# Kernel tuning notes

Hardware: AMD Instinct MI355X
Metric: run time of the kernel (lower is better)

## Reference

```python
import jax, jax.numpy as jnp
import numpy as np

N_USER = 50000
N_ITEM = 50000
E = 800000
D_IN = 256
H = 4
D_OUT = 32


def setup_inputs() -> dict:
    key = jax.random.key(0)
    ks = jax.random.split(key, 13)
    s = 0.05  # param init scale
    return {
        "feat_user": jax.random.normal(ks[0], (N_USER, D_IN), jnp.float32),
        "feat_item": jax.random.normal(ks[1], (N_ITEM, D_IN), jnp.float32),
        # relation 1: user -> item
        "src_r1": jax.random.randint(ks[2], (E,), 0, N_USER, jnp.int32),
        "dst_r1": jax.random.randint(ks[3], (E,), 0, N_ITEM, jnp.int32),
        # relation 2: item -> user
        "src_r2": jax.random.randint(ks[4], (E,), 0, N_ITEM, jnp.int32),
        "dst_r2": jax.random.randint(ks[5], (E,), 0, N_USER, jnp.int32),
        "fc_r1": jax.random.normal(ks[6], (D_IN, H * D_OUT), jnp.float32) * s,
        "attn_l_r1": jax.random.normal(ks[7], (H, D_OUT), jnp.float32) * s,
        "attn_r_r1": jax.random.normal(ks[8], (H, D_OUT), jnp.float32) * s,
        "fc_r2": jax.random.normal(ks[9], (D_IN, H * D_OUT), jnp.float32) * s,
        "attn_l_r2": jax.random.normal(ks[10], (H, D_OUT), jnp.float32) * s,
        "attn_r_r2": jax.random.normal(ks[11], (H, D_OUT), jnp.float32) * s,
        "loop_weight": jax.random.normal(ks[12], (D_IN, D_OUT), jnp.float32) * s,
    }


def _gat_conv(feat_src, feat_dst, src, dst, fc, attn_l, attn_r, n_dst):
    """DGL-style GATConv: LeakyReLU(0.2) scores, edge softmax over dst, scatter-sum, elu."""
    hs = (feat_src @ fc).reshape(-1, H, D_OUT)  # (Nsrc, H, D)
    hd = (feat_dst @ fc).reshape(-1, H, D_OUT)  # (Ndst, H, D)
    el = jnp.sum(hs * attn_l, axis=-1)  # (Nsrc, H)
    er = jnp.sum(hd * attn_r, axis=-1)  # (Ndst, H)
    e = jax.nn.leaky_relu(el[src] + er[dst], 0.2)  # (E, H)
    # numerically stable segment softmax over dst neighborhoods
    emax = jax.ops.segment_max(e, dst, num_segments=n_dst)  # (Ndst, H)
    emax = jnp.where(jnp.isfinite(emax), emax, 0.0)  # zero-in-degree guard
    ex = jnp.exp(e - emax[dst])  # (E, H)
    denom = jax.ops.segment_sum(ex, dst, num_segments=n_dst)  # (Ndst, H)
    msg = ex[:, :, None] * hs[src]  # (E, H, D)
    agg = jax.ops.segment_sum(msg, dst, num_segments=n_dst)  # (Ndst, H, D)
    out = agg / jnp.maximum(denom, 1e-9)[:, :, None]
    return jax.nn.elu(out)


def reference(feat_user, feat_item, src_r1, dst_r1, src_r2, dst_r2,
              fc_r1, attn_l_r1, attn_r_r1, fc_r2, attn_l_r2, attn_r_r2,
              loop_weight):
    # HeteroGraphConv: each dst ntype receives one relation here (sum-agg trivial)
    h_item = _gat_conv(feat_user, feat_item, src_r1, dst_r1,
                       fc_r1, attn_l_r1, attn_r_r1, N_ITEM)
    h_user = _gat_conv(feat_item, feat_user, src_r2, dst_r2,
                       fc_r2, attn_l_r2, attn_r_r2, N_USER)
    # self-loop fusion + wrapper activation (dropout=0 is identity)
    h_item = jax.nn.elu(h_item + (feat_item @ loop_weight)[:, None, :])
    h_user = jax.nn.elu(h_user + (feat_user @ loop_weight)[:, None, :])
    return jnp.stack([h_user, h_item])  # (2, 50000, H, D_OUT)
```

## Files before the change

### kernel.cpp

```cpp
#include <hip/hip_runtime.h>
#include <hip/hip_bf16.h>
#include <cstdint>

#define NU 50000
#define NI 50000
#define NN 50000
#define EE 800000
#define DIN 256
#define NH 4
#define DOUT 32
#define HD 128
#define WC 176
#define NB 196
#define NBR 200
#define NBLK 400
#define EPB 4000
#define SCAP 6144
#define PACKB 352

typedef __attribute__((ext_vector_type(8))) short short8;
typedef __attribute__((ext_vector_type(4))) float f32x4;
typedef __attribute__((ext_vector_type(2))) float f32x2;

__device__ __forceinline__ float leakyf(float x){ return x > 0.f ? x : 0.2f*x; }
__device__ __forceinline__ float eluf(float x){ return x > 0.f ? x : __expf(x) - 1.f; }
__device__ __forceinline__ unsigned short f2bf(float x){
  unsigned u = __float_as_uint(x);
  return (unsigned short)((u + 0x7FFFu + ((u >> 16) & 1u)) >> 16);
}
__device__ __forceinline__ float bf2f(unsigned short b){
  return __uint_as_float(((unsigned)b) << 16);
}
__device__ __forceinline__ float bflo(unsigned r){ return __uint_as_float(r << 16); }
__device__ __forceinline__ float bfhi(unsigned r){ return __uint_as_float(r & 0xffff0000u); }
__device__ __forceinline__ unsigned pk2(float x, float y){
  __hip_bfloat162 b = __float22bfloat162_rn(make_float2(x, y));
  union { __hip_bfloat162 b2; unsigned u; } c; c.b2 = b; return c.u;
}
__device__ __forceinline__ unsigned char f2fp8(float v){
  int pk = __builtin_amdgcn_cvt_pk_fp8_f32(v, v, 0, false);
  return (unsigned char)(pk & 0xff);
}

__global__ __launch_bounds__(256) void pack_bhist_k(
    const float* __restrict__ fc_r1, const float* __restrict__ al_r1,
    const float* __restrict__ ar_r1,
    const float* __restrict__ fc_r2, const float* __restrict__ al_r2,
    const float* __restrict__ ar_r2,
    const float* __restrict__ loopw,
    unsigned short* __restrict__ WtU, unsigned short* __restrict__ WtI,
    const int* __restrict__ d1, const int* __restrict__ d2,
    int* __restrict__ bhist) {
  __shared__ int hcnt[NB];
  int b = blockIdx.x;
  if (b < PACKB) {
    int side = b >= (PACKB/2);
    int bb = side ? b - (PACKB/2) : b;
    const float* fc_a = side ? fc_r2 : fc_r1;
    const float* al_a = side ? al_r2 : al_r1;
    const float* fc_b = side ? fc_r1 : fc_r2;
    const float* ar_b = side ? ar_r1 : ar_r2;
    unsigned short* Wt = side ? WtI : WtU;
    int t = bb*256 + threadIdx.x;
    if (t >= WC*DIN) return;
    int c = t >> 8, k = t & 255;
    float v = 0.f;
    if (c < HD) v = fc_a[k*HD + c];
    else if (c < HD+DOUT) v = loopw[k*DOUT + (c-HD)];
    else if (c < HD+DOUT+NH) {
      int h = c - (HD+DOUT); float s = 0.f;
      for (int dd = 0; dd < DOUT; ++dd) s += fc_a[k*HD + h*DOUT + dd] * al_a[h*DOUT + dd];
      v = s;
    } else if (c < HD+DOUT+2*NH) {
      int h = c - (HD+DOUT+NH); float s = 0.f;
      for (int dd = 0; dd < DOUT; ++dd) s += fc_b[k*HD + h*DOUT + dd] * ar_b[h*DOUT + dd];
      v = s;
    }
    Wt[t] = f2bf(v);
  } else {
    int blk = b - PACKB;
    int t = threadIdx.x;
    for (int i = t; i < NB; i += 256) hcnt[i] = 0;
    __syncthreads();
    int rel = blk >= NBR;
    const int* dd = rel ? d2 : d1;
    int e0 = (rel ? blk - NBR : blk) * EPB;
    for (int i = t; i < EPB; i += 256) atomicAdd(&hcnt[dd[e0+i] >> 8], 1);
    __syncthreads();
    for (int i = t; i < NB; i += 256) bhist[blk*NB + i] = hcnt[i];
  }
}

__global__ __launch_bounds__(512) void gemm_mfma(const float* __restrict__ Au,
                                                 const float* __restrict__ Ai,
                                                 const unsigned short* __restrict__ WtUp,
                                                 const unsigned short* __restrict__ WtIp,
                                                 unsigned char* __restrict__ hsbU8,
                                                 unsigned char* __restrict__ hsbI8,
                                                 unsigned short* __restrict__ loopbU,
                                                 unsigned short* __restrict__ loopbI,
                                                 unsigned short* __restrict__ elbU,
                                                 unsigned short* __restrict__ elbI,
                                                 float* __restrict__ erbU,
                                                 float* __restrict__ erbI) {
  int side = blockIdx.y;
  const float* A = side ? Ai : Au;
  const unsigned short* Wt = side ? WtIp : WtUp;
  unsigned char* hsb8 = side ? hsbI8 : hsbU8;
  unsigned short* loopb = side ? loopbI : loopbU;
  unsigned short* elb = side ? elbI : elbU;
  float* erb = side ? erbI : erbU;
  const int M = NN;

  __shared__ __align__(16) unsigned short As[2][128*40];
  __shared__ __align__(16) unsigned short Ws[2][176*40];
  int t = threadIdx.x;
  int bm = blockIdx.x * 128;
  int w = t >> 6, l = t & 63;
  int r16 = l & 15, g4 = l >> 4;
  f32x4 acc[11];
  #pragma unroll
  for (int f = 0; f < 11; ++f) acc[f] = (f32x4){0.f,0.f,0.f,0.f};

  int arow = t >> 2, aoff = (t & 3) * 8;
  int gr = bm + arow;
  int wc0 = t >> 2, woff0 = (t & 3) * 8;
  int wc1 = (t + 512) >> 2, woff1 = (t & 3) * 8;

  float4 a0, a1;
  uint4 wa, wb;
  auto loadT = [&](int k0) {
    a0 = make_float4(0.f,0.f,0.f,0.f); a1 = a0;
    if (gr < M) {
      const float* ap = A + (size_t)gr*DIN + k0 + aoff;
      a0 = *(const float4*)ap; a1 = *(const float4*)(ap + 4);
    }
    wa = *(const uint4*)(Wt + wc0*DIN + k0 + woff0);
    if (t < 192) wb = *(const uint4*)(Wt + wc1*DIN + k0 + woff1);
  };
  auto storeT = [&](int buf) {
    uint4 pk;
    pk.x = pk2(a0.x, a0.y); pk.y = pk2(a0.z, a0.w);
    pk.z = pk2(a1.x, a1.y); pk.w = pk2(a1.z, a1.w);
    *(uint4*)&As[buf][arow*40 + aoff] = pk;
    *(uint4*)&Ws[buf][wc0*40 + woff0] = wa;
    if (t < 192) *(uint4*)&Ws[buf][wc1*40 + woff1] = wb;
  };

  loadT(0);
  storeT(0);
  #pragma unroll
  for (int kt = 0; kt < 8; ++kt) {
    int cur = kt & 1;
    if (kt < 7) loadT((kt + 1) * 32);
    __syncthreads();
    short8 a = *(const short8*)&As[cur][(w*16 + r16)*40 + g4*8];
    #pragma unroll
    for (int f = 0; f < 11; ++f) {
      short8 b = *(const short8*)&Ws[cur][(f*16 + r16)*40 + g4*8];
      acc[f] = __builtin_amdgcn_mfma_f32_16x16x32_bf16(a, b, acc[f], 0, 0, 0);
    }
    if (kt < 7) storeT(cur ^ 1);
  }
  #pragma unroll
  for (int f = 0; f < 11; ++f) {
    int c = f*16 + r16;
    #pragma unroll
    for (int r = 0; r < 4; ++r) {
      int row = bm + w*16 + g4*4 + r;
      if (row >= M) continue;
      float v = acc[f][r];
      if (c < HD) hsb8[(size_t)row*HD + c] = f2fp8(v);
      else if (c < HD+DOUT) loopb[(size_t)row*DOUT + (c-HD)] = f2bf(v);
      else if (c < HD+DOUT+NH) elb[(size_t)row*NH + (c-(HD+DOUT))] = f2bf(v);
      else if (c < HD+DOUT+2*NH) erb[(size_t)row*NH + (c-(HD+DOUT+NH))] = v;
    }
  }
}

__global__ __launch_bounds__(256) void btot_k(const int* __restrict__ bhist,
                                              int* __restrict__ bucketbase,
                                              int* __restrict__ offs) {
  int rel = blockIdx.x, t = threadIdx.x;
  int tot = 0;
  if (t < NB)
    for (int blk = 0; blk < NBR; ++blk) tot += bhist[(rel*NBR + blk)*NB + t];
  int lane = t & 63, wv = t >> 6;
  __shared__ int ws[4];
  int x = tot;
  #pragma unroll
  for (int st = 1; st < 64; st <<= 1) { int y = __shfl_up(x, st); if (lane >= st) x += y; }
  if (lane == 63) ws[wv] = x;
  __syncthreads();
  int add = 0;
  for (int ww = 0; ww < wv; ++ww) add += ws[ww];
  int exc = x - tot + add;
  if (t < NB) bucketbase[rel*(NB+1) + t] = exc;
  if (t == 0) {
    bucketbase[rel*(NB+1) + NB] = EE;
    offs[rel*(NN+1) + NN] = EE;
  }
}

__global__ __launch_bounds__(256) void bscan_k(const int* __restrict__ bucketbase,
                                               int* __restrict__ bhist) {
  int gb = blockIdx.x, t = threadIdx.x;
  int rel = gb >= NB, b = rel ? gb - NB : gb;
  int base = rel*EE + bucketbase[rel*(NB+1) + b];
  int v = (t < NBR) ? bhist[(rel*NBR + t)*NB + b] : 0;
  int lane = t & 63, wv = t >> 6;
  __shared__ int ws[4];
  int x = v;
  #pragma unroll
  for (int st = 1; st < 64; st <<= 1) { int y = __shfl_up(x, st); if (lane >= st) x += y; }
  if (lane == 63) ws[wv] = x;
  __syncthreads();
  int add = base;
  for (int ww = 0; ww < wv; ++ww) add += ws[ww];
  int exc = x - v + add;
  if (t < NBR) bhist[(rel*NBR + t)*NB + b] = exc;
}

__global__ __launch_bounds__(256) void bscat_k(const int* __restrict__ s1, const int* __restrict__ d1,
                                               const int* __restrict__ s2, const int* __restrict__ d2,
                                               const int* __restrict__ bhist,
                                               unsigned* __restrict__ binned) {
  __shared__ int cur[NB];
  int blk = blockIdx.x, t = threadIdx.x;
  int rel = blk >= NBR;
  const int* ssrc = rel ? s2 : s1;
  const int* dd   = rel ? d2 : d1;
  int e0 = (rel ? blk - NBR : blk) * EPB;
  for (int i = t; i < NB; i += 256) cur[i] = bhist[blk*NB + i];
  __syncthreads();
  for (int i = t; i < EPB; i += 256) {
    int d = dd[e0+i], s = ssrc[e0+i];
    int pos = atomicAdd(&cur[d >> 8], 1);
    binned[pos] = (unsigned)s | ((unsigned)(d & 255) << 16);
  }
}

__global__ __launch_bounds__(256) void fine_k(const unsigned* __restrict__ binned,
                                              const int* __restrict__ bucketbase,
                                              int* __restrict__ offs,
                                              unsigned short* __restrict__ sorted1,
                                              unsigned short* __restrict__ sorted2) {
  __shared__ int cnt[256];
  __shared__ int cur[256];
  __shared__ int ws[4];
  __shared__ unsigned short stag[SCAP];
  int b = blockIdx.x, rel = blockIdx.y, t = threadIdx.x;
  unsigned short* sorted = rel ? sorted2 : sorted1;
  int d0 = b << 8;
  int nd = min(256, NN - d0);
  int base = bucketbase[rel*(NB+1) + b];
  int total = bucketbase[rel*(NB+1) + b + 1] - base;
  cnt[t] = 0;
  __syncthreads();
  const unsigned* srcp = binned + (size_t)rel*EE + base;
  for (int i = t; i < total; i += 256) atomicAdd(&cnt[srcp[i] >> 16], 1);
  __syncthreads();
  int v = cnt[t];
  int lane = t & 63, wv = t >> 6;
  int x = v;
  #pragma unroll
  for (int st = 1; st < 64; st <<= 1) { int y = __shfl_up(x, st); if (lane >= st) x += y; }
  if (lane == 63) ws[wv] = x;
  __syncthreads();
  int add = 0;
  for (int ww = 0; ww < wv; ++ww) add += ws[ww];
  int exc = x - v + add;
  cur[t] = exc;
  if (t < nd) offs[rel*(NN+1) + d0 + t] = base + exc;
  __syncthreads();
  for (int i = t; i < total; i += 256) {
    unsigned e = srcp[i];
    int pos = atomicAdd(&cur[e >> 16], 1);
    if (pos < SCAP) stag[pos] = (unsigned short)(e & 0xffffu);
  }
  __syncthreads();
  for (int i = t; i < total; i += 256)
    sorted[base + i] = stag[i];
}

__global__ __launch_bounds__(256) void weight_k(const unsigned short* __restrict__ elbU,
                                                const unsigned short* __restrict__ elbI,
                                                const float* __restrict__ erbU,
                                                const float* __restrict__ erbI,
                                                const int* __restrict__ offs,
                                                const unsigned short* __restrict__ sorted1,
                                                const unsigned short* __restrict__ sorted2,
                                                unsigned short* __restrict__ w1,
                                                unsigned short* __restrict__ w2) {
  int gw = (blockIdx.x*blockDim.x + threadIdx.x) >> 6;
  if (gw >= 2*NN) return;
  int rel = gw >= NN;
  int d = rel ? gw - NN : gw;
  const unsigned short* el_src = rel ? elbI : elbU;
  const float*          er_dst = rel ? erbU : erbI;
  const int*   of = offs + rel*(NN+1);
  const unsigned short* ss = rel ? sorted2 : sorted1;
  unsigned short* wb = rel ? w2 : w1;
  int beg = of[d], end = of[d+1];
  if (beg >= end) return;
  int l = threadIdx.x & 63, h = l >> 4, q = l & 15;
  float er = er_dst[(size_t)d*NH + h];
  float e_cache[4];
  float mx = -1e30f;
  int nch = 0;
  for (int p0 = beg; p0 < end; p0 += 16, ++nch) {
    int p = p0 + q;
    float e = -1e30f;
    if (p < end) {
      int s = ss[p];
      e = leakyf(bf2f(el_src[(size_t)s*NH + h]) + er);
    }
    if (nch < 4) e_cache[nch] = e;
    mx = fmaxf(mx, e);
  }
  #pragma unroll
  for (int st = 1; st < 16; st <<= 1) mx = fmaxf(mx, __shfl_xor(mx, st));
  float dnp = 0.f;
  int c = 0;
  for (int p0 = beg; p0 < end; p0 += 16, ++c) {
    int p = p0 + q;
    float e;
    if (c < 4) e = e_cache[c];
    else {
      e = -1e30f;
      if (p < end) { int s = ss[p]; e = leakyf(bf2f(el_src[(size_t)s*NH + h]) + er); }
    }
    float ex = (p < end) ? __expf(e - mx) : 0.f;
    if (c < 4) e_cache[c] = ex;
    dnp += ex;
  }
  #pragma unroll
  for (int st = 1; st < 16; st <<= 1) dnp += __shfl_xor(dnp, st);
  float rdn = 1.f / dnp;
  c = 0;
  for (int p0 = beg; p0 < end; p0 += 16, ++c) {
    int p = p0 + q;
    if (p < end) {
      float ex;
      if (c < 4) ex = e_cache[c];
      else { int s = ss[p]; ex = __expf(leakyf(bf2f(el_src[(size_t)s*NH + h]) + er) - mx); }
      wb[(size_t)p*4 + h] = f2bf(ex * rdn);
    }
  }
}

__global__ __launch_bounds__(256) void agg_k(const unsigned char* __restrict__ hsbU8,
                                             const unsigned char* __restrict__ hsbI8,
                                             const unsigned short* __restrict__ loopbU,
                                             const unsigned short* __restrict__ loopbI,
                                             const unsigned short* __restrict__ w1,
                                             const unsigned short* __restrict__ w2,
                                             const int* __restrict__ offs,
                                             const unsigned short* __restrict__ sorted1,
                                             const unsigned short* __restrict__ sorted2,
                                             float* __restrict__ out) {
  int gw = __builtin_amdgcn_readfirstlane((blockIdx.x*blockDim.x + threadIdx.x) >> 6);
  if (gw >= 2*NN) return;
  int rel = gw >= NN;
  int d = rel ? gw - NN : gw;
  const unsigned char* hsb8 = rel ? hsbI8 : hsbU8;
  const unsigned short* lpb = rel ? loopbU : loopbI;
  const unsigned short* wb = rel ? w2 : w1;
  const int*   of = offs + rel*(NN+1);
  const unsigned short* ss = rel ? sorted2 : sorted1;
  float* o = (rel ? out : out + (size_t)NN*HD) + (size_t)d*HD;
  int l = threadIdx.x & 63;
  int g = l >> 4, j = l & 15, h = j >> 2;
  int beg = of[d], end = of[d+1];
  float a0=0.f,a1=0.f,a2=0.f,a3=0.f,a4=0.f,a5=0.f,a6=0.f,a7=0.f;
  int p = beg;
  for (; p + 8 <= end; p += 8) {
    int sA = (int)ss[p + g];
    int sB = (int)ss[p + 4 + g];
    float wA = bf2f(wb[(size_t)(p + g)*4 + h]);
    float wB = bf2f(wb[(size_t)(p + 4 + g)*4 + h]);
    uint2 rA = *(const uint2*)&hsb8[(size_t)sA*HD + 8*j];
    uint2 rB = *(const uint2*)&hsb8[(size_t)sB*HD + 8*j];
    f32x2 f0 = __builtin_amdgcn_cvt_pk_f32_fp8(rA.x, false);
    f32x2 f1 = __builtin_amdgcn_cvt_pk_f32_fp8(rA.x, true);
    f32x2 f2 = __builtin_amdgcn_cvt_pk_f32_fp8(rA.y, false);
    f32x2 f3 = __builtin_amdgcn_cvt_pk_f32_fp8(rA.y, true);
    a0 = fmaf(wA, f0.x, a0); a1 = fmaf(wA, f0.y, a1);
    a2 = fmaf(wA, f1.x, a2); a3 = fmaf(wA, f1.y, a3);
    a4 = fmaf(wA, f2.x, a4); a5 = fmaf(wA, f2.y, a5);
    a6 = fmaf(wA, f3.x, a6); a7 = fmaf(wA, f3.y, a7);
    f32x2 g0 = __builtin_amdgcn_cvt_pk_f32_fp8(rB.x, false);
    f32x2 g1 = __builtin_amdgcn_cvt_pk_f32_fp8(rB.x, true);
    f32x2 g2 = __builtin_amdgcn_cvt_pk_f32_fp8(rB.y, false);
    f32x2 g3 = __builtin_amdgcn_cvt_pk_f32_fp8(rB.y, true);
    a0 = fmaf(wB, g0.x, a0); a1 = fmaf(wB, g0.y, a1);
    a2 = fmaf(wB, g1.x, a2); a3 = fmaf(wB, g1.y, a3);
    a4 = fmaf(wB, g2.x, a4); a5 = fmaf(wB, g2.y, a5);
    a6 = fmaf(wB, g3.x, a6); a7 = fmaf(wB, g3.y, a7);
  }
  for (; p < end; p += 4) {
    if (p + g < end) {
      int sA = (int)ss[p + g];
      float wA = bf2f(wb[(size_t)(p + g)*4 + h]);
      uint2 rA = *(const uint2*)&hsb8[(size_t)sA*HD + 8*j];
      f32x2 f0 = __builtin_amdgcn_cvt_pk_f32_fp8(rA.x, false);
      f32x2 f1 = __builtin_amdgcn_cvt_pk_f32_fp8(rA.x, true);
      f32x2 f2 = __builtin_amdgcn_cvt_pk_f32_fp8(rA.y, false);
      f32x2 f3 = __builtin_amdgcn_cvt_pk_f32_fp8(rA.y, true);
      a0 = fmaf(wA, f0.x, a0); a1 = fmaf(wA, f0.y, a1);
      a2 = fmaf(wA, f1.x, a2); a3 = fmaf(wA, f1.y, a3);
      a4 = fmaf(wA, f2.x, a4); a5 = fmaf(wA, f2.y, a5);
      a6 = fmaf(wA, f3.x, a6); a7 = fmaf(wA, f3.y, a7);
    }
  }
  a0 += __shfl_xor(a0, 16); a0 += __shfl_xor(a0, 32);
  a1 += __shfl_xor(a1, 16); a1 += __shfl_xor(a1, 32);
  a2 += __shfl_xor(a2, 16); a2 += __shfl_xor(a2, 32);
  a3 += __shfl_xor(a3, 16); a3 += __shfl_xor(a3, 32);
  a4 += __shfl_xor(a4, 16); a4 += __shfl_xor(a4, 32);
  a5 += __shfl_xor(a5, 16); a5 += __shfl_xor(a5, 32);
  a6 += __shfl_xor(a6, 16); a6 += __shfl_xor(a6, 32);
  a7 += __shfl_xor(a7, 16); a7 += __shfl_xor(a7, 32);
  if (g == 0) {
    uint4 lp = *(const uint4*)&lpb[(size_t)d*DOUT + 8*(j & 3)];
    float4 v0, v1;
    v0.x = eluf(eluf(a0) + bflo(lp.x)); v0.y = eluf(eluf(a1) + bfhi(lp.x));
    v0.z = eluf(eluf(a2) + bflo(lp.y)); v0.w = eluf(eluf(a3) + bfhi(lp.y));
    v1.x = eluf(eluf(a4) + bflo(lp.z)); v1.y = eluf(eluf(a5) + bfhi(lp.z));
    v1.z = eluf(eluf(a6) + bflo(lp.w)); v1.w = eluf(eluf(a7) + bfhi(lp.w));
    *(float4*)&o[8*j] = v0;
    *(float4*)&o[8*j + 4] = v1;
  }
}

extern "C" void kernel_launch(void* const* d_in, const int* in_sizes, int n_in,
                              void* d_out, int out_size, void* d_ws, size_t ws_size,
                              hipStream_t stream) {
  const float* feat_user  = (const float*)d_in[0];
  const float* feat_item  = (const float*)d_in[1];
  const int*   src_r1     = (const int*)d_in[2];
  const int*   dst_r1     = (const int*)d_in[3];
  const int*   src_r2     = (const int*)d_in[4];
  const int*   dst_r2     = (const int*)d_in[5];
  const float* fc_r1      = (const float*)d_in[6];
  const float* attn_l_r1  = (const float*)d_in[7];
  const float* attn_r_r1  = (const float*)d_in[8];
  const float* fc_r2      = (const float*)d_in[9];
  const float* attn_l_r2  = (const float*)d_in[10];
  const float* attn_r_r2  = (const float*)d_in[11];
  const float* loopw      = (const float*)d_in[12];

  float* out = (float*)d_out;

  char* ws = (char*)d_ws;
  unsigned short* WtU   = (unsigned short*)ws;            ws += WC*DIN*2;
  unsigned short* WtI   = (unsigned short*)ws;            ws += WC*DIN*2;
  unsigned char*  hsbU8 = (unsigned char*)ws;             ws += (size_t)NU*HD;
  unsigned char*  hsbI8 = (unsigned char*)ws;             ws += (size_t)NI*HD;
  unsigned short* loopbU= (unsigned short*)ws;            ws += (size_t)NU*DOUT*2;
  unsigned short* loopbI= (unsigned short*)ws;            ws += (size_t)NI*DOUT*2;
  unsigned short* elbU  = (unsigned short*)ws;            ws += (size_t)NU*NH*2;
  unsigned short* elbI  = (unsigned short*)ws;            ws += (size_t)NI*NH*2;
  float*          erbU  = (float*)ws;                     ws += (size_t)NU*NH*4;
  float*          erbI  = (float*)ws;                     ws += (size_t)NI*NH*4;
  int*            offs  = (int*)ws;                       ws += 2*(NN+1)*4;
  int*            bktb  = (int*)ws;                       ws += 2*(NB+1)*4;
  int*            bhist = (int*)ws;                       ws += (size_t)NBLK*NB*4;
  unsigned*       binned= (unsigned*)ws;                  ws += (size_t)2*EE*4;
  unsigned short* sorted1=(unsigned short*)ws;            ws += (size_t)EE*2;
  unsigned short* sorted2=(unsigned short*)ws;            ws += (size_t)EE*2;
  unsigned short* w1    = (unsigned short*)ws;            ws += (size_t)EE*NH*2;
  unsigned short* w2    = (unsigned short*)ws;            ws += (size_t)EE*NH*2;

  pack_bhist_k<<<PACKB + NBLK, 256, 0, stream>>>(fc_r1, attn_l_r1, attn_r_r1,
                                                 fc_r2, attn_l_r2, attn_r_r2,
                                                 loopw, WtU, WtI,
                                                 dst_r1, dst_r2, bhist);
  btot_k<<<2, 256, 0, stream>>>(bhist, bktb, offs);
  bscan_k<<<2*NB, 256, 0, stream>>>(bktb, bhist);
  bscat_k<<<NBLK, 256, 0, stream>>>(src_r1, dst_r1, src_r2, dst_r2, bhist, binned);
  fine_k<<<dim3(NB,2), 256, 0, stream>>>(binned, bktb, offs, sorted1, sorted2);

  gemm_mfma<<<dim3((NN+127)/128, 2), 512, 0, stream>>>(feat_user, feat_item, WtU, WtI,
                                                       hsbU8, hsbI8, loopbU, loopbI,
                                                       elbU, elbI, erbU, erbI);

  weight_k<<<(2*NN*64 + 255)/256, 256, 0, stream>>>(elbU, elbI, erbU, erbI,
                                                    offs, sorted1, sorted2, w1, w2);
  agg_k<<<(2*NN*64 + 255)/256, 256, 0, stream>>>(hsbU8, hsbI8, loopbU, loopbI, w1, w2,
                                                 offs, sorted1, sorted2, out);
}
```

Baseline: 158.3 us.

## Fuse edge-softmax weight kernel into aggregation using per-wave LDS weight buffer

```diff
diff --git a/kernel.cpp b/kernel.cpp
--- a/kernel.cpp
+++ b/kernel.cpp
@@ -17,6 +17,7 @@
 #define EPB 4000
 #define SCAP 6144
 #define PACKB 352
+#define WCAP 128
 
 typedef __attribute__((ext_vector_type(8))) short short8;
 typedef __attribute__((ext_vector_type(4))) float f32x4;
@@ -283,102 +284,92 @@
     sorted[base + i] = stag[i];
 }
 
-__global__ __launch_bounds__(256) void weight_k(const unsigned short* __restrict__ elbU,
-                                                const unsigned short* __restrict__ elbI,
-                                                const float* __restrict__ erbU,
-                                                const float* __restrict__ erbI,
-                                                const int* __restrict__ offs,
-                                                const unsigned short* __restrict__ sorted1,
-                                                const unsigned short* __restrict__ sorted2,
-                                                unsigned short* __restrict__ w1,
-                                                unsigned short* __restrict__ w2) {
-  int gw = (blockIdx.x*blockDim.x + threadIdx.x) >> 6;
-  if (gw >= 2*NN) return;
+__global__ __launch_bounds__(256) void agg_k(const unsigned char* __restrict__ hsbU8,
+                                             const unsigned char* __restrict__ hsbI8,
+                                             const unsigned short* __restrict__ loopbU,
+                                             const unsigned short* __restrict__ loopbI,
+                                             const unsigned short* __restrict__ elbU,
+                                             const unsigned short* __restrict__ elbI,
+                                             const float* __restrict__ erbU,
+                                             const float* __restrict__ erbI,
+                                             const int* __restrict__ offs,
+                                             const unsigned short* __restrict__ sorted1,
+                                             const unsigned short* __restrict__ sorted2,
+                                             float* __restrict__ out) {
+  __shared__ float wlds[4][WCAP*NH];
+  int wvid = threadIdx.x >> 6;
+  float* mywl = wlds[wvid];
+  int gw = __builtin_amdgcn_readfirstlane((blockIdx.x*blockDim.x + threadIdx.x) >> 6);
   int rel = gw >= NN;
   int d = rel ? gw - NN : gw;
+  const unsigned char* hsb8 = rel ? hsbI8 : hsbU8;
+  const unsigned short* lpb = rel ? loopbU : loopbI;
   const unsigned short* el_src = rel ? elbI : elbU;
   const float*          er_dst = rel ? erbU : erbI;
   const int*   of = offs + rel*(NN+1);
   const unsigned short* ss = rel ? sorted2 : sorted1;
-  unsigned short* wb = rel ? w2 : w1;
-  int beg = of[d], end = of[d+1];
-  if (beg >= end) return;
-  int l = threadIdx.x & 63, h = l >> 4, q = l & 15;
-  float er = er_dst[(size_t)d*NH + h];
-  float e_cache[4];
-  float mx = -1e30f;
-  int nch = 0;
-  for (int p0 = beg; p0 < end; p0 += 16, ++nch) {
-    int p = p0 + q;
-    float e = -1e30f;
-    if (p < end) {
-      int s = ss[p];
-      e = leakyf(bf2f(el_src[(size_t)s*NH + h]) + er);
-    }
-    if (nch < 4) e_cache[nch] = e;
-    mx = fmaxf(mx, e);
-  }
-  #pragma unroll
-  for (int st = 1; st < 16; st <<= 1) mx = fmaxf(mx, __shfl_xor(mx, st));
-  float dnp = 0.f;
-  int c = 0;
-  for (int p0 = beg; p0 < end; p0 += 16, ++c) {
-    int p = p0 + q;
-    float e;
-    if (c < 4) e = e_cache[c];
-    else {
-      e = -1e30f;
-      if (p < end) { int s = ss[p]; e = leakyf(bf2f(el_src[(size_t)s*NH + h]) + er); }
-    }
-    float ex = (p < end) ? __expf(e - mx) : 0.f;
-    if (c < 4) e_cache[c] = ex;
-    dnp += ex;
-  }
-  #pragma unroll
-  for (int st = 1; st < 16; st <<= 1) dnp += __shfl_xor(dnp, st);
-  float rdn = 1.f / dnp;
-  c = 0;
-  for (int p0 = beg; p0 < end; p0 += 16, ++c) {
-    int p = p0 + q;
-    if (p < end) {
-      float ex;
-      if (c < 4) ex = e_cache[c];
-      else { int s = ss[p]; ex = __expf(leakyf(bf2f(el_src[(size_t)s*NH + h]) + er) - mx); }
-      wb[(size_t)p*4 + h] = f2bf(ex * rdn);
-    }
-  }
-}
-
-__global__ __launch_bounds__(256) void agg_k(const unsigned char* __restrict__ hsbU8,
-                                             const unsigned char* __restrict__ hsbI8,
-                                             const unsigned short* __restrict__ loopbU,
-                                             const unsigned short* __restrict__ loopbI,
-                                             const unsigned short* __restrict__ w1,
-                                             const unsigned short* __restrict__ w2,
-                                             const int* __restrict__ offs,
-                                             const unsigned short* __restrict__ sorted1,
-                                             const unsigned short* __restrict__ sorted2,
-                                             float* __restrict__ out) {
-  int gw = __builtin_amdgcn_readfirstlane((blockIdx.x*blockDim.x + threadIdx.x) >> 6);
-  if (gw >= 2*NN) return;
-  int rel = gw >= NN;
-  int d = rel ? gw - NN : gw;
-  const unsigned char* hsb8 = rel ? hsbI8 : hsbU8;
-  const unsigned short* lpb = rel ? loopbU : loopbI;
-  const unsigned short* wb = rel ? w2 : w1;
-  const int*   of = offs + rel*(NN+1);
-  const unsigned short* ss = rel ? sorted2 : sorted1;
   float* o = (rel ? out : out + (size_t)NN*HD) + (size_t)d*HD;
   int l = threadIdx.x & 63;
+  int beg = of[d], end = of[d+1];
+  int deg = end - beg;
+
+  int hp = l >> 4, q = l & 15;
+  float mx = -1e30f, rdn = 0.f, er = 0.f;
+  if (deg > 0) {
+    er = er_dst[(size_t)d*NH + hp];
+    float e_cache[4];
+    int nch = 0;
+    for (int p0 = beg; p0 < end; p0 += 16, ++nch) {
+      int p = p0 + q;
+      float e = -1e30f;
+      if (p < end) {
+        int s = (int)ss[p];
+        e = leakyf(bf2f(el_src[(size_t)s*NH + hp]) + er);
+      }
+      if (nch < 4) e_cache[nch] = e;
+      mx = fmaxf(mx, e);
+    }
+    #pragma unroll
+    for (int st = 1; st < 16; st <<= 1) mx = fmaxf(mx, __shfl_xor(mx, st));
+    float dnp = 0.f;
+    int c = 0;
+    for (int p0 = beg; p0 < end; p0 += 16, ++c) {
+      int p = p0 + q;
+      float e;
+      if (c < 4) e = e_cache[c];
+      else {
+        e = -1e30f;
+        if (p < end) { int s = (int)ss[p]; e = leakyf(bf2f(el_src[(size_t)s*NH + hp]) + er); }
+      }
+      float ex = (p < end) ? __expf(e - mx) : 0.f;
+      if (c < 4) e_cache[c] = ex;
+      dnp += ex;
+    }
+    #pragma unroll
+    for (int st = 1; st < 16; st <<= 1) dnp += __shfl_xor(dnp, st);
+    rdn = 1.f / dnp;
+    c = 0;
+    for (int p0 = beg; p0 < end && c < (WCAP/16); p0 += 16, ++c) {
+      int p = p0 + q;
+      if (p < end) {
+        float ex;
+        if (c < 4) ex = e_cache[c];
+        else { int s = (int)ss[p]; ex = __expf(leakyf(bf2f(el_src[(size_t)s*NH + hp]) + er) - mx); }
+        mywl[(p - beg)*NH + hp] = ex * rdn;
+      }
+    }
+  }
+  asm volatile("s_waitcnt lgkmcnt(0)" ::: "memory");
+
   int g = l >> 4, j = l & 15, h = j >> 2;
-  int beg = of[d], end = of[d+1];
+  int fastend = (deg > WCAP) ? (beg + WCAP) : end;
   float a0=0.f,a1=0.f,a2=0.f,a3=0.f,a4=0.f,a5=0.f,a6=0.f,a7=0.f;
   int p = beg;
-  for (; p + 8 <= end; p += 8) {
+  for (; p + 8 <= fastend; p += 8) {
     int sA = (int)ss[p + g];
     int sB = (int)ss[p + 4 + g];
-    float wA = bf2f(wb[(size_t)(p + g)*4 + h]);
-    float wB = bf2f(wb[(size_t)(p + 4 + g)*4 + h]);
+    float wA = mywl[(p + g - beg)*NH + h];
+    float wB = mywl[(p + 4 + g - beg)*NH + h];
     uint2 rA = *(const uint2*)&hsb8[(size_t)sA*HD + 8*j];
     uint2 rB = *(const uint2*)&hsb8[(size_t)sB*HD + 8*j];
     f32x2 f0 = __builtin_amdgcn_cvt_pk_f32_fp8(rA.x, false);
@@ -398,10 +389,10 @@
     a4 = fmaf(wB, g2.x, a4); a5 = fmaf(wB, g2.y, a5);
     a6 = fmaf(wB, g3.x, a6); a7 = fmaf(wB, g3.y, a7);
   }
-  for (; p < end; p += 4) {
-    if (p + g < end) {
+  for (; p < fastend; p += 4) {
+    if (p + g < fastend) {
       int sA = (int)ss[p + g];
-      float wA = bf2f(wb[(size_t)(p + g)*4 + h]);
+      float wA = mywl[(p + g - beg)*NH + h];
       uint2 rA = *(const uint2*)&hsb8[(size_t)sA*HD + 8*j];
       f32x2 f0 = __builtin_amdgcn_cvt_pk_f32_fp8(rA.x, false);
       f32x2 f1 = __builtin_amdgcn_cvt_pk_f32_fp8(rA.x, true);
@@ -411,6 +402,26 @@
       a2 = fmaf(wA, f1.x, a2); a3 = fmaf(wA, f1.y, a3);
       a4 = fmaf(wA, f2.x, a4); a5 = fmaf(wA, f2.y, a5);
       a6 = fmaf(wA, f3.x, a6); a7 = fmaf(wA, f3.y, a7);
+    }
+  }
+  if (end > fastend) {
+    float mxg  = __shfl(mx,  h*16);
+    float rdng = __shfl(rdn, h*16);
+    float erg  = __shfl(er,  h*16);
+    for (int pp = fastend; pp < end; ++pp) {
+      int s = __builtin_amdgcn_readfirstlane((int)ss[pp]);
+      float wv_ = __expf(leakyf(bf2f(el_src[(size_t)s*NH + h]) + erg) - mxg) * rdng;
+      if (g == 0) {
+        uint2 r = *(const uint2*)&hsb8[(size_t)s*HD + 8*j];
+        f32x2 f0 = __builtin_amdgcn_cvt_pk_f32_fp8(r.x, false);
+        f32x2 f1 = __builtin_amdgcn_cvt_pk_f32_fp8(r.x, true);
+        f32x2 f2 = __builtin_amdgcn_cvt_pk_f32_fp8(r.y, false);
+        f32x2 f3 = __builtin_amdgcn_cvt_pk_f32_fp8(r.y, true);
+        a0 = fmaf(wv_, f0.x, a0); a1 = fmaf(wv_, f0.y, a1);
+        a2 = fmaf(wv_, f1.x, a2); a3 = fmaf(wv_, f1.y, a3);
+        a4 = fmaf(wv_, f2.x, a4); a5 = fmaf(wv_, f2.y, a5);
+        a6 = fmaf(wv_, f3.x, a6); a7 = fmaf(wv_, f3.y, a7);
+      }
     }
   }
   a0 += __shfl_xor(a0, 16); a0 += __shfl_xor(a0, 32);
@@ -469,8 +480,6 @@
   unsigned*       binned= (unsigned*)ws;                  ws += (size_t)2*EE*4;
   unsigned short* sorted1=(unsigned short*)ws;            ws += (size_t)EE*2;
   unsigned short* sorted2=(unsigned short*)ws;            ws += (size_t)EE*2;
-  unsigned short* w1    = (unsigned short*)ws;            ws += (size_t)EE*NH*2;
-  unsigned short* w2    = (unsigned short*)ws;            ws += (size_t)EE*NH*2;
 
   pack_bhist_k<<<PACKB + NBLK, 256, 0, stream>>>(fc_r1, attn_l_r1, attn_r_r1,
                                                  fc_r2, attn_l_r2, attn_r_r2,
@@ -485,8 +494,7 @@
                                                        hsbU8, hsbI8, loopbU, loopbI,
                                                        elbU, elbI, erbU, erbI);
 
-  weight_k<<<(2*NN*64 + 255)/256, 256, 0, stream>>>(elbU, elbI, erbU, erbI,
-                                                    offs, sorted1, sorted2, w1, w2);
-  agg_k<<<(2*NN*64 + 255)/256, 256, 0, stream>>>(hsbU8, hsbI8, loopbU, loopbI, w1, w2,
-                                                 offs, sorted1, sorted2, out);
-}
+  agg_k<<<(2*NN*64)/256, 256, 0, stream>>>(hsbU8, hsbI8, loopbU, loopbI,
+                                           elbU, elbI, erbU, erbI,
+                                           offs, sorted1, sorted2, out);
+}
```

Result: faster. 147.3 us (-7.0%).
